# Kernel tuning notes

Hardware: AMD Instinct MI355X
Metric: run time of the kernel (lower is better)

Reference implementation:

```python
import jax, jax.numpy as jnp
import numpy as np

FEATURE_LIST = [222, 27, 373, 283, 26, 7]
EMB_HID = 6
TN, UN, TF = 2000, 50000, 16


def setup_inputs() -> dict:
    key = jax.random.key(0)
    ks = jax.random.split(key, 4 + len(FEATURE_LIST))
    T_static = jax.random.normal(ks[0], (TN, TF), dtype=jnp.float32)
    # per-column categorical indices, each in-range for its table
    cols = [jax.random.randint(jax.random.fold_in(ks[1], i), (UN,), 0, sz)
            for i, sz in enumerate(FEATURE_LIST)]
    U_static = jnp.stack(cols, axis=1).astype(jnp.int64)  # [UN, 6]
    team_user_matrix = jax.random.randint(ks[2], (TN, UN), 0, 2, dtype=jnp.int32)
    inp = {"T_static": T_static, "U_static": U_static,
           "team_user_matrix": team_user_matrix}
    # embedding tables, xavier_uniform with gain=sqrt(2)
    for i, sz in enumerate(FEATURE_LIST):
        bound = np.sqrt(2.0) * np.sqrt(6.0 / (sz + EMB_HID))
        inp[f"emb{i}"] = jax.random.uniform(ks[3 + i], (sz, EMB_HID),
                                            minval=-bound, maxval=bound,
                                            dtype=jnp.float32)
    return inp


def reference(T_static, U_static, team_user_matrix,
              emb0, emb1, emb2, emb3, emb4, emb5):
    tables = [emb0, emb1, emb2, emb3, emb4, emb5]
    # gather per-feature embeddings and concat -> [UN, 6*emb_hid]
    U_emb = jnp.concatenate(
        [t[U_static[:, i]] for i, t in enumerate(tables)], axis=-1)
    mask = (team_user_matrix == 1).astype(U_emb.dtype)        # [TN, UN]
    counts = jnp.sum(mask, axis=1, keepdims=True)             # [TN, 1]
    # masked mean over each team's users == (mask @ U_emb) / counts
    T_emb = jnp.matmul(mask, U_emb) / counts                  # [TN, 36]
    return jnp.concatenate([T_static, T_emb], axis=-1)        # [TN, TF+36]
```

## Files before the change

### kernel.cpp

```cpp
#include <hip/hip_runtime.h>
#include <hip/hip_bf16.h>

#define TN 2000
#define UN 50000
#define TF 16
#define NCOL 48
#define UNP 50016
#define KSTEPS 1563
#define KFULL 1562
#define KCHUNKS 48
#define SPC 33
#define MTILES 125

typedef __attribute__((ext_vector_type(8))) short short8;
typedef __attribute__((ext_vector_type(4))) float f32x4;
typedef __attribute__((ext_vector_type(4))) int i32x4;

__device__ inline unsigned short f2bf(float f) {
    unsigned int x = __float_as_uint(f);
    x += 0x7FFFu + ((x >> 16) & 1u);
    return (unsigned short)(x >> 16);
}

__global__ void build_uembT(const int* __restrict__ U,
                            const float* __restrict__ e0, const float* __restrict__ e1,
                            const float* __restrict__ e2, const float* __restrict__ e3,
                            const float* __restrict__ e4, const float* __restrict__ e5,
                            unsigned short* __restrict__ BS) {
    int u = blockIdx.x * 256 + threadIdx.x;
    int c = blockIdx.y;
    if (u >= UNP) return;
    unsigned short val = 0;
    if (u < UN) {
        if (c < 36) {
            int f = c / 6, h = c - f * 6;
            const float* t = (f == 0) ? e0 : (f == 1) ? e1 : (f == 2) ? e2
                           : (f == 3) ? e3 : (f == 4) ? e4 : e5;
            int idx = U[u * 6 + f];
            val = f2bf(t[idx * 6 + h]);
        } else if (c == 36) {
            val = 0x3F80;
        }
    }
    int ks   = u >> 5;
    int g    = (u & 31) >> 3;
    int j    = u & 7;
    int lane = g * 16 + (c & 15);
    int tile = c >> 4;
    BS[(((size_t)ks * 3 + tile) * 64 + lane) * 8 + j] = val;
}

__device__ inline short8 mask_to_bf16(i32x4 v0, i32x4 v1) {
    union { short8 s; int i[4]; } a;
    a.i[0] = ((v0.x == 1) ? 0x3F80 : 0) | ((v0.y == 1) ? 0x3F800000 : 0);
    a.i[1] = ((v0.z == 1) ? 0x3F80 : 0) | ((v0.w == 1) ? 0x3F800000 : 0);
    a.i[2] = ((v1.x == 1) ? 0x3F80 : 0) | ((v1.y == 1) ? 0x3F800000 : 0);
    a.i[3] = ((v1.z == 1) ? 0x3F80 : 0) | ((v1.w == 1) ? 0x3F800000 : 0);
    return a.s;
}

__global__ __launch_bounds__(256) void masked_gemm(
        const int* __restrict__ mask, const unsigned short* __restrict__ BS,
        float* __restrict__ partial) {
    int wave = threadIdx.x >> 6;
    int lane = threadIdx.x & 63;
    int mtile = blockIdx.x * 4 + wave;
    if (mtile >= MTILES) return;
    int m0 = mtile * 16;
    int r  = lane & 15;
    int g8 = (lane >> 4) * 8;
    int ky = blockIdx.y;

    int ks0 = ky * SPC;
    int ks1 = ks0 + SPC; if (ks1 > KSTEPS) ks1 = KSTEPS;
    int ksf = (ks1 < KFULL) ? ks1 : KFULL;

    f32x4 acc0 = {0.f, 0.f, 0.f, 0.f};
    f32x4 acc1 = {0.f, 0.f, 0.f, 0.f};
    f32x4 acc2 = {0.f, 0.f, 0.f, 0.f};

    const int* arow = mask + (size_t)(m0 + r) * UN + g8;
    const short8* bs = (const short8*)BS + lane;

    #pragma unroll 3
    for (int ks = ks0; ks < ksf; ++ks) {
        int gk = ks * 32;
        const i32x4* p = (const i32x4*)(arow + gk);
        i32x4 v0 = p[0], v1 = p[1];
        short8 a  = mask_to_bf16(v0, v1);
        short8 f0 = bs[(size_t)(ks * 3    ) * 64];
        short8 f1 = bs[(size_t)(ks * 3 + 1) * 64];
        short8 f2 = bs[(size_t)(ks * 3 + 2) * 64];
        acc0 = __builtin_amdgcn_mfma_f32_16x16x32_bf16(a, f0, acc0, 0, 0, 0);
        acc1 = __builtin_amdgcn_mfma_f32_16x16x32_bf16(a, f1, acc1, 0, 0, 0);
        acc2 = __builtin_amdgcn_mfma_f32_16x16x32_bf16(a, f2, acc2, 0, 0, 0);
    }
    if (ks1 > KFULL) {
        int tk = KFULL * 32;
        short8 a = {0,0,0,0,0,0,0,0};
        if (g8 < 16) {
            const i32x4* p = (const i32x4*)(arow + tk);
            i32x4 v0 = p[0], v1 = p[1];
            a = mask_to_bf16(v0, v1);
        }
        short8 t0 = bs[(size_t)(KFULL * 3    ) * 64];
        short8 t1 = bs[(size_t)(KFULL * 3 + 1) * 64];
        short8 t2 = bs[(size_t)(KFULL * 3 + 2) * 64];
        acc0 = __builtin_amdgcn_mfma_f32_16x16x32_bf16(a, t0, acc0, 0, 0, 0);
        acc1 = __builtin_amdgcn_mfma_f32_16x16x32_bf16(a, t1, acc1, 0, 0, 0);
        acc2 = __builtin_amdgcn_mfma_f32_16x16x32_bf16(a, t2, acc2, 0, 0, 0);
    }

    int row0 = m0 + (lane >> 4) * 4;
    int col  = lane & 15;
    #pragma unroll
    for (int reg = 0; reg < 4; ++reg) {
        size_t rb = ((size_t)(row0 + reg) * KCHUNKS + ky) * NCOL;
        partial[rb + col]      = acc0[reg];
        partial[rb + col + 16] = acc1[reg];
        if (col < 5)
            partial[rb + col + 32] = acc2[reg];
    }
}

__global__ void finalize(const float* __restrict__ T_static,
                         const float* __restrict__ partial,
                         float* __restrict__ out) {
    int t = blockIdx.x;
    int c = threadIdx.x;
    if (c >= TF + 36) return;
    float v;
    if (c < TF) {
        v = T_static[(size_t)t * TF + c];
    } else {
        int n = c - TF;
        const float* base = partial + (size_t)t * KCHUNKS * NCOL;
        float s = 0.f, cnt = 0.f;
        #pragma unroll 6
        for (int ky = 0; ky < KCHUNKS; ++ky) {
            s   += base[ky * NCOL + n];
            cnt += base[ky * NCOL + 36];
        }
        v = s / cnt;
    }
    out[(size_t)t * (TF + 36) + c] = v;
}

extern "C" void kernel_launch(void* const* d_in, const int* in_sizes, int n_in,
                              void* d_out, int out_size, void* d_ws, size_t ws_size,
                              hipStream_t stream) {
    const float* T_static = (const float*)d_in[0];
    const int*   U_static = (const int*)d_in[1];
    const int*   mask     = (const int*)d_in[2];
    const float* e0 = (const float*)d_in[3];
    const float* e1 = (const float*)d_in[4];
    const float* e2 = (const float*)d_in[5];
    const float* e3 = (const float*)d_in[6];
    const float* e4 = (const float*)d_in[7];
    const float* e5 = (const float*)d_in[8];
    float* out = (float*)d_out;

    unsigned short* BS = (unsigned short*)d_ws;
    size_t bs_bytes = (size_t)KSTEPS * 3 * 64 * 8 * sizeof(unsigned short);
    float* partial = (float*)((char*)d_ws + bs_bytes);

    build_uembT<<<dim3((UNP + 255) / 256, NCOL), dim3(256), 0, stream>>>(
        U_static, e0, e1, e2, e3, e4, e5, BS);
    masked_gemm<<<dim3(32, KCHUNKS), dim3(256), 0, stream>>>(mask, BS, partial);
    finalize<<<dim3(TN), dim3(64), 0, stream>>>(T_static, partial, out);
}
```

Before: 574.4 us.

## Process two M-tiles per wave to reuse B fragments and simplify mask conversion

Each wave now computes two 16-row tiles of the team/user mask, M-tiles t and t+64, with six accumulators. The loaded embedding B fragments are shared across both, and the grid's x dimension is halved. The mask-to-bf16 conversion uses multiplies instead of compare/select, which is only equivalent when mask entries are exactly 0 or 1. Together these aim to cut redundant B loads and ALU work and raise memory-level parallelism per wave, at the cost of more registers and fewer resident waves.

```diff
diff --git a/kernel.cpp b/kernel.cpp
--- a/kernel.cpp
+++ b/kernel.cpp
@@ -51,11 +51,11 @@
 }
 
 __device__ inline short8 mask_to_bf16(i32x4 v0, i32x4 v1) {
-    union { short8 s; int i[4]; } a;
-    a.i[0] = ((v0.x == 1) ? 0x3F80 : 0) | ((v0.y == 1) ? 0x3F800000 : 0);
-    a.i[1] = ((v0.z == 1) ? 0x3F80 : 0) | ((v0.w == 1) ? 0x3F800000 : 0);
-    a.i[2] = ((v1.x == 1) ? 0x3F80 : 0) | ((v1.y == 1) ? 0x3F800000 : 0);
-    a.i[3] = ((v1.z == 1) ? 0x3F80 : 0) | ((v1.w == 1) ? 0x3F800000 : 0);
+    union { short8 s; unsigned int i[4]; } a;
+    a.i[0] = (unsigned)v0.x * 0x3F80u + (unsigned)v0.y * 0x3F800000u;
+    a.i[1] = (unsigned)v0.z * 0x3F80u + (unsigned)v0.w * 0x3F800000u;
+    a.i[2] = (unsigned)v1.x * 0x3F80u + (unsigned)v1.y * 0x3F800000u;
+    a.i[3] = (unsigned)v1.z * 0x3F80u + (unsigned)v1.w * 0x3F800000u;
     return a.s;
 }
 
@@ -64,9 +64,10 @@
         float* __restrict__ partial) {
     int wave = threadIdx.x >> 6;
     int lane = threadIdx.x & 63;
-    int mtile = blockIdx.x * 4 + wave;
-    if (mtile >= MTILES) return;
-    int m0 = mtile * 16;
+    int slot = blockIdx.x * 4 + wave;
+    int mt0 = slot;
+    int mt1 = slot + 64;
+    bool two = (mt1 < MTILES);
     int r  = lane & 15;
     int g8 = (lane >> 4) * 8;
     int ky = blockIdx.y;
@@ -75,51 +76,89 @@
     int ks1 = ks0 + SPC; if (ks1 > KSTEPS) ks1 = KSTEPS;
     int ksf = (ks1 < KFULL) ? ks1 : KFULL;
 
-    f32x4 acc0 = {0.f, 0.f, 0.f, 0.f};
-    f32x4 acc1 = {0.f, 0.f, 0.f, 0.f};
-    f32x4 acc2 = {0.f, 0.f, 0.f, 0.f};
-
-    const int* arow = mask + (size_t)(m0 + r) * UN + g8;
+    f32x4 acc00 = {0,0,0,0}, acc01 = {0,0,0,0}, acc02 = {0,0,0,0};
+    f32x4 acc10 = {0,0,0,0}, acc11 = {0,0,0,0}, acc12 = {0,0,0,0};
+
+    const int* arow0 = mask + (size_t)(mt0 * 16 + r) * UN + g8;
+    const int* arow1 = arow0 + (size_t)64 * 16 * UN;
     const short8* bs = (const short8*)BS + lane;
 
-    #pragma unroll 3
-    for (int ks = ks0; ks < ksf; ++ks) {
-        int gk = ks * 32;
-        const i32x4* p = (const i32x4*)(arow + gk);
-        i32x4 v0 = p[0], v1 = p[1];
-        short8 a  = mask_to_bf16(v0, v1);
-        short8 f0 = bs[(size_t)(ks * 3    ) * 64];
-        short8 f1 = bs[(size_t)(ks * 3 + 1) * 64];
-        short8 f2 = bs[(size_t)(ks * 3 + 2) * 64];
-        acc0 = __builtin_amdgcn_mfma_f32_16x16x32_bf16(a, f0, acc0, 0, 0, 0);
-        acc1 = __builtin_amdgcn_mfma_f32_16x16x32_bf16(a, f1, acc1, 0, 0, 0);
-        acc2 = __builtin_amdgcn_mfma_f32_16x16x32_bf16(a, f2, acc2, 0, 0, 0);
+    if (two) {
+        #pragma unroll 3
+        for (int ks = ks0; ks < ksf; ++ks) {
+            int gk = ks * 32;
+            const i32x4* p0 = (const i32x4*)(arow0 + gk);
+            const i32x4* p1 = (const i32x4*)(arow1 + gk);
+            i32x4 u0 = p0[0], u1 = p0[1];
+            i32x4 w0 = p1[0], w1 = p1[1];
+            short8 a0 = mask_to_bf16(u0, u1);
+            short8 a1 = mask_to_bf16(w0, w1);
+            short8 f0 = bs[(size_t)(ks * 3    ) * 64];
+            short8 f1 = bs[(size_t)(ks * 3 + 1) * 64];
+            short8 f2 = bs[(size_t)(ks * 3 + 2) * 64];
+            acc00 = __builtin_amdgcn_mfma_f32_16x16x32_bf16(a0, f0, acc00, 0, 0, 0);
+            acc01 = __builtin_amdgcn_mfma_f32_16x16x32_bf16(a0, f1, acc01, 0, 0, 0);
+            acc02 = __builtin_amdgcn_mfma_f32_16x16x32_bf16(a0, f2, acc02, 0, 0, 0);
+            acc10 = __builtin_amdgcn_mfma_f32_16x16x32_bf16(a1, f0, acc10, 0, 0, 0);
+            acc11 = __builtin_amdgcn_mfma_f32_16x16x32_bf16(a1, f1, acc11, 0, 0, 0);
+            acc12 = __builtin_amdgcn_mfma_f32_16x16x32_bf16(a1, f2, acc12, 0, 0, 0);
+        }
+    } else {
+        #pragma unroll 3
+        for (int ks = ks0; ks < ksf; ++ks) {
+            int gk = ks * 32;
+            const i32x4* p0 = (const i32x4*)(arow0 + gk);
+            i32x4 u0 = p0[0], u1 = p0[1];
+            short8 a0 = mask_to_bf16(u0, u1);
+            short8 f0 = bs[(size_t)(ks * 3    ) * 64];
+            short8 f1 = bs[(size_t)(ks * 3 + 1) * 64];
+            short8 f2 = bs[(size_t)(ks * 3 + 2) * 64];
+            acc00 = __builtin_amdgcn_mfma_f32_16x16x32_bf16(a0, f0, acc00, 0, 0, 0);
+            acc01 = __builtin_amdgcn_mfma_f32_16x16x32_bf16(a0, f1, acc01, 0, 0, 0);
+            acc02 = __builtin_amdgcn_mfma_f32_16x16x32_bf16(a0, f2, acc02, 0, 0, 0);
+        }
     }
     if (ks1 > KFULL) {
         int tk = KFULL * 32;
-        short8 a = {0,0,0,0,0,0,0,0};
+        short8 a0 = {0,0,0,0,0,0,0,0}, a1 = {0,0,0,0,0,0,0,0};
         if (g8 < 16) {
-            const i32x4* p = (const i32x4*)(arow + tk);
-            i32x4 v0 = p[0], v1 = p[1];
-            a = mask_to_bf16(v0, v1);
+            const i32x4* p0 = (const i32x4*)(arow0 + tk);
+            a0 = mask_to_bf16(p0[0], p0[1]);
+            if (two) {
+                const i32x4* p1 = (const i32x4*)(arow1 + tk);
+                a1 = mask_to_bf16(p1[0], p1[1]);
+            }
         }
         short8 t0 = bs[(size_t)(KFULL * 3    ) * 64];
         short8 t1 = bs[(size_t)(KFULL * 3 + 1) * 64];
         short8 t2 = bs[(size_t)(KFULL * 3 + 2) * 64];
-        acc0 = __builtin_amdgcn_mfma_f32_16x16x32_bf16(a, t0, acc0, 0, 0, 0);
-        acc1 = __builtin_amdgcn_mfma_f32_16x16x32_bf16(a, t1, acc1, 0, 0, 0);
-        acc2 = __builtin_amdgcn_mfma_f32_16x16x32_bf16(a, t2, acc2, 0, 0, 0);
-    }
-
-    int row0 = m0 + (lane >> 4) * 4;
-    int col  = lane & 15;
+        acc00 = __builtin_amdgcn_mfma_f32_16x16x32_bf16(a0, t0, acc00, 0, 0, 0);
+        acc01 = __builtin_amdgcn_mfma_f32_16x16x32_bf16(a0, t1, acc01, 0, 0, 0);
+        acc02 = __builtin_amdgcn_mfma_f32_16x16x32_bf16(a0, t2, acc02, 0, 0, 0);
+        if (two) {
+            acc10 = __builtin_amdgcn_mfma_f32_16x16x32_bf16(a1, t0, acc10, 0, 0, 0);
+            acc11 = __builtin_amdgcn_mfma_f32_16x16x32_bf16(a1, t1, acc11, 0, 0, 0);
+            acc12 = __builtin_amdgcn_mfma_f32_16x16x32_bf16(a1, t2, acc12, 0, 0, 0);
+        }
+    }
+
+    int rbase = (lane >> 4) * 4;
+    int col   = lane & 15;
     #pragma unroll
     for (int reg = 0; reg < 4; ++reg) {
-        size_t rb = ((size_t)(row0 + reg) * KCHUNKS + ky) * NCOL;
-        partial[rb + col]      = acc0[reg];
-        partial[rb + col + 16] = acc1[reg];
-        if (col < 5)
-            partial[rb + col + 32] = acc2[reg];
+        size_t rb = ((size_t)(mt0 * 16 + rbase + reg) * KCHUNKS + ky) * NCOL;
+        partial[rb + col]      = acc00[reg];
+        partial[rb + col + 16] = acc01[reg];
+        if (col < 5) partial[rb + col + 32] = acc02[reg];
+    }
+    if (two) {
+        #pragma unroll
+        for (int reg = 0; reg < 4; ++reg) {
+            size_t rb = ((size_t)(mt1 * 16 + rbase + reg) * KCHUNKS + ky) * NCOL;
+            partial[rb + col]      = acc10[reg];
+            partial[rb + col + 16] = acc11[reg];
+            if (col < 5) partial[rb + col + 32] = acc12[reg];
+        }
     }
 }
 
@@ -166,6 +205,6 @@
 
     build_uembT<<<dim3((UNP + 255) / 256, NCOL), dim3(256), 0, stream>>>(
         U_static, e0, e1, e2, e3, e4, e5, BS);
-    masked_gemm<<<dim3(32, KCHUNKS), dim3(256), 0, stream>>>(mask, BS, partial);
+    masked_gemm<<<dim3(16, KCHUNKS), dim3(256), 0, stream>>>(mask, BS, partial);
     finalize<<<dim3(TN), dim3(64), 0, stream>>>(T_static, partial, out);
 }
```

New measurement: 567.6 us. Within noise of the previous version (-1.2%).
